# Kernel tuning notes

Measured on AMD Instinct MI355X. Metric: run time of the kernel, lower is better.

## Reference

```python
import jax, jax.numpy as jnp
import numpy as np

HEADS = 4
HID = 64
IN_DIM = 128
N_WIRES, N_TERM, N_ACT = 50, 20, 10
NEG_SLOPE = 0.2


def gat_conv(x, src, dst, ea, W, We, a_src, a_dst, a_edge, bias, concat):
    """PyG GATConv with edge features, add_self_loops=True, fill_value='mean'."""
    N = x.shape[0]
    H, F = a_src.shape
    # --- add self loops; self-loop edge_attr = mean of incoming edge_attr ---
    deg = jax.ops.segment_sum(jnp.ones((ea.shape[0],), x.dtype), dst, num_segments=N)
    loop_attr = jax.ops.segment_sum(ea, dst, num_segments=N) / jnp.maximum(deg, 1.0)[:, None]
    ar = jnp.arange(N)
    src = jnp.concatenate([src, ar])
    dst = jnp.concatenate([dst, ar])
    ea = jnp.concatenate([ea, loop_attr], axis=0)
    # --- linear transforms ---
    h = (x @ W).reshape(N, H, F)                      # [N,H,F]
    a_s = jnp.einsum('nhf,hf->nh', h, a_src)          # [N,H]
    a_d = jnp.einsum('nhf,hf->nh', h, a_dst)
    he = (ea @ We).reshape(-1, H, F)                  # [E2,H,F]
    a_e = jnp.einsum('ehf,hf->eh', he, a_edge)        # [E2,H]
    # --- attention logits + softmax over edges grouped by destination ---
    alpha = jax.nn.leaky_relu(a_s[src] + a_d[dst] + a_e, negative_slope=NEG_SLOPE)
    amax = jax.ops.segment_max(alpha, dst, num_segments=N)
    ex = jnp.exp(alpha - amax[dst])
    denom = jax.ops.segment_sum(ex, dst, num_segments=N)
    alpha = ex / (denom[dst] + 1e-16)                 # [E2,H]
    # --- message passing: gather src feats, weight, scatter-sum to dst ---
    out = jax.ops.segment_sum(h[src] * alpha[..., None], dst, num_segments=N)  # [N,H,F]
    out = out.reshape(N, H * F) if concat else out.mean(axis=1)
    return out + bias


def setup_inputs() -> dict:
    key = jax.random.key(0)
    ks = jax.random.split(key, 24)
    N, E = 20000, 320000
    x = jax.random.normal(ks[0], (N, IN_DIM), jnp.float32)
    edge_index = jax.random.randint(ks[1], (2, E), 0, N, dtype=jnp.int64)
    edge_attr = jax.random.normal(ks[2], (E, 2), jnp.float32)
    s = 0.1
    p = {
        'W1': jax.random.normal(ks[3], (IN_DIM, HEADS * HID)) * s,
        'We1': jax.random.normal(ks[4], (2, HEADS * HID)) * s,
        'as1': jax.random.normal(ks[5], (HEADS, HID)) * s,
        'ad1': jax.random.normal(ks[6], (HEADS, HID)) * s,
        'ae1': jax.random.normal(ks[7], (HEADS, HID)) * s,
        'b1': jnp.zeros((HEADS * HID,), jnp.float32),
        'W2': jax.random.normal(ks[8], (HEADS * HID, HEADS * HID)) * s,
        'We2': jax.random.normal(ks[9], (2, HEADS * HID)) * s,
        'as2': jax.random.normal(ks[10], (HEADS, HID)) * s,
        'ad2': jax.random.normal(ks[11], (HEADS, HID)) * s,
        'ae2': jax.random.normal(ks[12], (HEADS, HID)) * s,
        'b2': jnp.zeros((HID,), jnp.float32),
        'Ww': jax.random.normal(ks[13], (HID, N_WIRES)) * s,
        'bw': jnp.zeros((N_WIRES,), jnp.float32),
        'Wt': jax.random.normal(ks[14], (HID, N_TERM)) * s,
        'bt': jnp.zeros((N_TERM,), jnp.float32),
        'Wa': jax.random.normal(ks[15], (HID, N_ACT)) * s,
        'ba': jnp.zeros((N_ACT,), jnp.float32),
    }
    return {'x': x, 'edge_index': edge_index, 'edge_attr': edge_attr, **p}


def reference(x, edge_index, edge_attr, W1, We1, as1, ad1, ae1, b1,
              W2, We2, as2, ad2, ae2, b2, Ww, bw, Wt, bt, Wa, ba):
    src, dst = edge_index[0], edge_index[1]
    h = jax.nn.elu(gat_conv(x, src, dst, edge_attr, W1, We1, as1, ad1, ae1, b1, True))
    h = jax.nn.elu(gat_conv(h, src, dst, edge_attr, W2, We2, as2, ad2, ae2, b2, False))
    wire_logits = h @ Ww + bw
    terminal_logits = h @ Wt + bt
    action_logits = h @ Wa + ba
    return (wire_logits, terminal_logits, action_logits)
```

## Files before the change

kernel.cpp:

```cpp
#include <hip/hip_runtime.h>
#include <math.h>

#define N_NODES 20000
#define N_EDGES 320000
#define D1      256
#define WCAP    128
#define NPB     10385
#define NDEG    1250
#define NWALL   32

typedef __attribute__((ext_vector_type(8))) short    bf16x8;
typedef __attribute__((ext_vector_type(4))) float    f32x4;
typedef __attribute__((ext_vector_type(8))) unsigned short u16x8;

__device__ inline float wred_sum(float v) {
#pragma unroll
  for (int o = 32; o > 0; o >>= 1) v += __shfl_xor(v, o, 64);
  return v;
}
__device__ inline float wred_max(float v) {
#pragma unroll
  for (int o = 32; o > 0; o >>= 1) v = fmaxf(v, __shfl_xor(v, o, 64));
  return v;
}

__device__ inline unsigned short f2b(float v) {
  unsigned u = __float_as_uint(v);
  unsigned r = (u + 0x7fffu + ((u >> 16) & 1u)) >> 16;
  return (unsigned short)r;
}
__device__ inline float b2f(unsigned short h) {
  return __uint_as_float(((unsigned)h) << 16);
}

__device__ inline int fr(const int* __restrict__ rp, const int* __restrict__ boff, int j) {
  return j ? rp[j] + boff[(j - 1) >> 10] : 0;
}

__global__ __launch_bounds__(256) void k_prep(
    const float* __restrict__ x, unsigned short* __restrict__ xh,
    const float* __restrict__ W1, unsigned short* __restrict__ WT1h,
    unsigned short* __restrict__ WT1l,
    const float* __restrict__ W2, unsigned short* __restrict__ WT2h,
    unsigned short* __restrict__ WT2l,
    const float* __restrict__ We1, const float* __restrict__ ae1,
    const float* __restrict__ We2, const float* __restrict__ ae2,
    float* __restrict__ qb,
    const int* __restrict__ ei, int* __restrict__ deg,
    const float* __restrict__ Ww, const float* __restrict__ Wt,
    const float* __restrict__ Wa,
    const float* __restrict__ bw, const float* __restrict__ bt,
    const float* __restrict__ ba,
    unsigned short* __restrict__ WallTh, unsigned short* __restrict__ WallTl,
    float* __restrict__ biasAll) {
  int bid = blockIdx.x, t = threadIdx.x;
  if (bid < 10000) {
    int i = bid * 256 + t;
    xh[i] = f2b(x[i]);
  } else if (bid < 10128) {
    int i = (bid - 10000) * 256 + t;
    int k = i >> 8, n = i & 255;
    float v = W1[i];
    unsigned short h = f2b(v);
    WT1h[n * 128 + k] = h;
    WT1l[n * 128 + k] = f2b(v - b2f(h));
  } else if (bid < 10384) {
    int i = (bid - 10128) * 256 + t;
    int k = i >> 8, n = i & 255;
    float v = W2[i];
    unsigned short h = f2b(v);
    WT2h[n * 256 + k] = h;
    WT2l[n * 256 + k] = f2b(v - b2f(h));
  } else if (bid == 10384) {
    int lane = t & 63, w = t >> 6;
    const float* We = (w >> 1) ? We2 : We1;
    const float* ae = (w >> 1) ? ae2 : ae1;
    int c = w & 1;
#pragma unroll
    for (int h = 0; h < 4; h++) {
      float p = We[c * D1 + h * 64 + lane] * ae[h * 64 + lane];
      p = wred_sum(p);
      if (lane == 0) qb[(w >> 1) * 8 + c * 4 + h] = p;
    }
    if (t < 80) biasAll[t] = (t < 50) ? bw[t] : (t < 70) ? bt[t - 50] : ba[t - 70];
  } else if (bid < NPB + NDEG) {
    int e = (bid - NPB) * 256 + t;
    if (e < N_EDGES) atomicAdd(&deg[ei[N_EDGES + e]], 1);
  } else {
    int i = (bid - NPB - NDEG) * 256 + t;
    int j = i >> 6, f = i & 63;
    float v = 0.f;
    if (j < 50)      v = Ww[f * 50 + j];
    else if (j < 70) v = Wt[f * 20 + (j - 50)];
    else if (j < 80) v = Wa[f * 10 + (j - 70)];
    unsigned short h = f2b(v);
    WallTh[j * 64 + f] = h;
    WallTl[j * 64 + f] = f2b(v - b2f(h));
  }
}

__global__ __launch_bounds__(1024) void k_scan1(const int* __restrict__ deg,
                                                int* __restrict__ rowptr,
                                                int* __restrict__ bsum, int N) {
  __shared__ int wsum[16];
  int t = threadIdx.x, lane = t & 63, wid = t >> 6;
  int i = blockIdx.x * 1024 + t;
  int v = (i < N) ? deg[i] : 0;
  int sc = v;
#pragma unroll
  for (int o = 1; o < 64; o <<= 1) {
    int u = __shfl_up(sc, o, 64);
    if (lane >= o) sc += u;
  }
  if (lane == 63) wsum[wid] = sc;
  __syncthreads();
  if (wid == 0 && lane < 16) {
    int x = wsum[lane];
#pragma unroll
    for (int o = 1; o < 16; o <<= 1) {
      int u = __shfl_up(x, o, 64);
      if (lane >= o) x += u;
    }
    wsum[lane] = x;
  }
  __syncthreads();
  int off = wid ? wsum[wid - 1] : 0;
  if (i < N) rowptr[i + 1] = off + sc;
  if (t == 0) bsum[blockIdx.x] = wsum[15];
}

__global__ void k_scan2(const int* __restrict__ bsum, int* __restrict__ boff, int nb) {
  int lane = threadIdx.x;
  int v = (lane < nb) ? bsum[lane] : 0;
  int sc = v;
#pragma unroll
  for (int o = 1; o < 64; o <<= 1) {
    int u = __shfl_up(sc, o, 64);
    if (lane >= o) sc += u;
  }
  if (lane < nb) boff[lane] = sc - v;
}

__global__ void k_scatter(const int* __restrict__ ei, const float* __restrict__ ea,
                          const int* __restrict__ rowptr, const int* __restrict__ boff,
                          int* __restrict__ fill, int* __restrict__ src_s,
                          float* __restrict__ ea_s) {
  int p = blockIdx.x * blockDim.x + threadIdx.x;
  if (p >= N_EDGES) return;
  int s = ei[p], d = ei[N_EDGES + p];
  float e0 = ea[p * 2], e1 = ea[p * 2 + 1];
  int pos = fr(rowptr, boff, d) + atomicAdd(&fill[d], 1);
  src_s[pos] = s;
  ea_s[pos * 2] = e0; ea_s[pos * 2 + 1] = e1;
}

#define LDK 40
__global__ __launch_bounds__(256) void k_gemm_mfma(
    const unsigned short* __restrict__ Ah,
    const unsigned short* __restrict__ BTh, const unsigned short* __restrict__ BTl,
    unsigned short* __restrict__ Chi,
    const float* __restrict__ asw, const float* __restrict__ adw,
    float* __restrict__ asb, float* __restrict__ adb,
    int M, int K) {
  __shared__ unsigned short sAh[128 * LDK];
  __shared__ unsigned short sBh[128 * LDK], sBl[128 * LDK];
  int tid = threadIdx.x;
  int lane = tid & 63, wid = tid >> 6;
  int wr = wid >> 1, wc = wid & 1;
  int row0 = blockIdx.y * 128, col0 = blockIdx.x * 128;
  int aRow = wr * 64, bRow = wc * 64;

  f32x4 acc[4][4];
#pragma unroll
  for (int i = 0; i < 4; i++)
#pragma unroll
    for (int j = 0; j < 4; j++) acc[i][j] = (f32x4){0.f, 0.f, 0.f, 0.f};

  int c0i = tid * 2;
  int r0 = c0i >> 2, ko0 = (c0i & 3) * 8;
  int c1i = tid * 2 + 1;
  int r1 = c1i >> 2, ko1 = (c1i & 3) * 8;

  int q8 = (lane >> 4) * 8;
  int rsel = lane & 15;

  for (int k0 = 0; k0 < K; k0 += 32) {
    u16x8 z = {0, 0, 0, 0, 0, 0, 0, 0};
    int ga0 = row0 + r0, ga1 = row0 + r1;
    u16x8 vah0 = (ga0 < M) ? *(const u16x8*)&Ah[(size_t)ga0 * K + k0 + ko0] : z;
    u16x8 vah1 = (ga1 < M) ? *(const u16x8*)&Ah[(size_t)ga1 * K + k0 + ko1] : z;
    u16x8 vbh0 = *(const u16x8*)&BTh[(size_t)(col0 + r0) * K + k0 + ko0];
    u16x8 vbl0 = *(const u16x8*)&BTl[(size_t)(col0 + r0) * K + k0 + ko0];
    u16x8 vbh1 = *(const u16x8*)&BTh[(size_t)(col0 + r1) * K + k0 + ko1];
    u16x8 vbl1 = *(const u16x8*)&BTl[(size_t)(col0 + r1) * K + k0 + ko1];
    *(u16x8*)&sAh[r0 * LDK + ko0] = vah0;
    *(u16x8*)&sAh[r1 * LDK + ko1] = vah1;
    *(u16x8*)&sBh[r0 * LDK + ko0] = vbh0;
    *(u16x8*)&sBl[r0 * LDK + ko0] = vbl0;
    *(u16x8*)&sBh[r1 * LDK + ko1] = vbh1;
    *(u16x8*)&sBl[r1 * LDK + ko1] = vbl1;
    __syncthreads();

    bf16x8 fah[4], fbh[4], fbl[4];
#pragma unroll
    for (int i = 0; i < 4; i++) {
      int ar = aRow + i * 16 + rsel;
      int br = bRow + i * 16 + rsel;
      fah[i] = *(const bf16x8*)&sAh[ar * LDK + q8];
      fbh[i] = *(const bf16x8*)&sBh[br * LDK + q8];
      fbl[i] = *(const bf16x8*)&sBl[br * LDK + q8];
    }
#pragma unroll
    for (int i = 0; i < 4; i++)
#pragma unroll
      for (int j = 0; j < 4; j++) {
        acc[i][j] = __builtin_amdgcn_mfma_f32_16x16x32_bf16(fah[i], fbh[j], acc[i][j], 0, 0, 0);
        acc[i][j] = __builtin_amdgcn_mfma_f32_16x16x32_bf16(fah[i], fbl[j], acc[i][j], 0, 0, 0);
      }
    __syncthreads();
  }

  int rq = (lane >> 4) * 4;
  int head = (col0 + bRow) >> 6;
  float sa[4], sd[4];
#pragma unroll
  for (int j = 0; j < 4; j++) {
    sa[j] = asw[head * 64 + j * 16 + rsel];
    sd[j] = adw[head * 64 + j * 16 + rsel];
  }
#pragma unroll
  for (int i = 0; i < 4; i++) {
#pragma unroll
    for (int j = 0; j < 4; j++) {
      int gcol = col0 + bRow + j * 16 + rsel;
#pragma unroll
      for (int r = 0; r < 4; r++) {
        int grow = row0 + aRow + i * 16 + rq + r;
        if (grow < M) Chi[(size_t)grow * D1 + gcol] = f2b(acc[i][j][r]);
      }
    }
#pragma unroll
    for (int r = 0; r < 4; r++) {
      float ps = 0.f, pd = 0.f;
#pragma unroll
      for (int j = 0; j < 4; j++) {
        ps = fmaf(acc[i][j][r], sa[j], ps);
        pd = fmaf(acc[i][j][r], sd[j], pd);
      }
#pragma unroll
      for (int o = 1; o < 16; o <<= 1) {
        ps += __shfl_xor(ps, o, 64);
        pd += __shfl_xor(pd, o, 64);
      }
      int grow = row0 + aRow + i * 16 + rq + r;
      if ((lane & 15) == 0 && grow < M) {
        asb[grow * 4 + head] = ps;
        adb[grow * 4 + head] = pd;
      }
    }
  }
}

__global__ __launch_bounds__(256) void k_heads_mfma(
    const unsigned short* __restrict__ Ah, const unsigned short* __restrict__ Al,
    const unsigned short* __restrict__ BTh, const unsigned short* __restrict__ BTl,
    const float* __restrict__ biasAll, float* __restrict__ out, int M) {
  __shared__ unsigned short sAh[128 * LDK], sAl[128 * LDK];
  __shared__ unsigned short sBh[128 * LDK], sBl[128 * LDK];
  const int K = 64;
  int tid = threadIdx.x;
  int lane = tid & 63, wid = tid >> 6;
  int wr = wid >> 1, wc = wid & 1;
  int row0 = blockIdx.x * 128;
  int aRow = wr * 64, bRow = wc * 64;

  f32x4 acc[4][4];
#pragma unroll
  for (int i = 0; i < 4; i++)
#pragma unroll
    for (int j = 0; j < 4; j++) acc[i][j] = (f32x4){0.f, 0.f, 0.f, 0.f};

  int c0i = tid * 2;
  int r0 = c0i >> 2, ko0 = (c0i & 3) * 8;
  int c1i = tid * 2 + 1;
  int r1 = c1i >> 2, ko1 = (c1i & 3) * 8;
  int q8 = (lane >> 4) * 8;
  int rsel = lane & 15;

  for (int k0 = 0; k0 < K; k0 += 32) {
    u16x8 z = {0, 0, 0, 0, 0, 0, 0, 0};
    int ga0 = row0 + r0, ga1 = row0 + r1;
    u16x8 vah0 = (ga0 < M) ? *(const u16x8*)&Ah[(size_t)ga0 * K + k0 + ko0] : z;
    u16x8 val0 = (ga0 < M) ? *(const u16x8*)&Al[(size_t)ga0 * K + k0 + ko0] : z;
    u16x8 vah1 = (ga1 < M) ? *(const u16x8*)&Ah[(size_t)ga1 * K + k0 + ko1] : z;
    u16x8 val1 = (ga1 < M) ? *(const u16x8*)&Al[(size_t)ga1 * K + k0 + ko1] : z;
    u16x8 vbh0 = *(const u16x8*)&BTh[(size_t)r0 * K + k0 + ko0];
    u16x8 vbl0 = *(const u16x8*)&BTl[(size_t)r0 * K + k0 + ko0];
    u16x8 vbh1 = *(const u16x8*)&BTh[(size_t)r1 * K + k0 + ko1];
    u16x8 vbl1 = *(const u16x8*)&BTl[(size_t)r1 * K + k0 + ko1];
    *(u16x8*)&sAh[r0 * LDK + ko0] = vah0;
    *(u16x8*)&sAl[r0 * LDK + ko0] = val0;
    *(u16x8*)&sAh[r1 * LDK + ko1] = vah1;
    *(u16x8*)&sAl[r1 * LDK + ko1] = val1;
    *(u16x8*)&sBh[r0 * LDK + ko0] = vbh0;
    *(u16x8*)&sBl[r0 * LDK + ko0] = vbl0;
    *(u16x8*)&sBh[r1 * LDK + ko1] = vbh1;
    *(u16x8*)&sBl[r1 * LDK + ko1] = vbl1;
    __syncthreads();

    bf16x8 fah[4], fal[4], fbh[4], fbl[4];
#pragma unroll
    for (int i = 0; i < 4; i++) {
      int ar = aRow + i * 16 + rsel;
      int br = bRow + i * 16 + rsel;
      fah[i] = *(const bf16x8*)&sAh[ar * LDK + q8];
      fal[i] = *(const bf16x8*)&sAl[ar * LDK + q8];
      fbh[i] = *(const bf16x8*)&sBh[br * LDK + q8];
      fbl[i] = *(const bf16x8*)&sBl[br * LDK + q8];
    }
#pragma unroll
    for (int i = 0; i < 4; i++)
#pragma unroll
      for (int j = 0; j < 4; j++) {
        acc[i][j] = __builtin_amdgcn_mfma_f32_16x16x32_bf16(fah[i], fbh[j], acc[i][j], 0, 0, 0);
        acc[i][j] = __builtin_amdgcn_mfma_f32_16x16x32_bf16(fah[i], fbl[j], acc[i][j], 0, 0, 0);
        acc[i][j] = __builtin_amdgcn_mfma_f32_16x16x32_bf16(fal[i], fbh[j], acc[i][j], 0, 0, 0);
      }
    __syncthreads();
  }

  int rq = (lane >> 4) * 4;
#pragma unroll
  for (int j = 0; j < 4; j++) {
    int gcol = bRow + j * 16 + rsel;
    if (gcol < 80) {
      float bj = biasAll[gcol];
      float* op; int cols, jj;
      if (gcol < 50)      { op = out;                 cols = 50; jj = gcol; }
      else if (gcol < 70) { op = out + N_NODES * 50;  cols = 20; jj = gcol - 50; }
      else                { op = out + N_NODES * 70;  cols = 10; jj = gcol - 70; }
#pragma unroll
      for (int i = 0; i < 4; i++) {
#pragma unroll
        for (int r = 0; r < 4; r++) {
          int grow = row0 + aRow + i * 16 + rq + r;
          if (grow < M) op[(size_t)grow * cols + jj] = acc[i][j][r] + bj;
        }
      }
    }
  }
}

template <bool CONCAT>
__global__ __launch_bounds__(256) void k_aggregate(
    const unsigned short* __restrict__ feath,
    const int* __restrict__ rowptr, const int* __restrict__ boff,
    const int* __restrict__ src_s, const float* __restrict__ ea_s,
    const float* __restrict__ asb, const float* __restrict__ adb,
    const float* __restrict__ q, const float* __restrict__ bias,
    unsigned short* __restrict__ outh,
    unsigned short* __restrict__ outf_h, unsigned short* __restrict__ outf_l) {
  __shared__ float slog[4][4][WCAP];
  __shared__ int   ssrc[4][WCAP];
  int t = threadIdx.x, lane = t & 63, w = t >> 6;
  int n = blockIdx.x * 4 + w;
  int b = fr(rowptr, boff, n);
  int e = fr(rowptr, boff, n + 1);
  int deg = e - b;

  float4 qv0 = *(const float4*)q;
  float4 qv1 = *(const float4*)(q + 4);
  float4 ad4 = *(const float4*)&adb[(size_t)n * 4];
  float4 asn = *(const float4*)&asb[(size_t)n * 4];

  if (deg <= WCAP) {
    float lv[2][4];
    float e0acc = 0.f, e1acc = 0.f;
#pragma unroll
    for (int p = 0; p < 2; p++) {
      int j = lane + p * 64;
      float l0 = -1e30f, l1 = -1e30f, l2 = -1e30f, l3 = -1e30f;
      if (j < deg) {
        int s = src_s[b + j];
        float4 as4 = *(const float4*)&asb[(size_t)s * 4];
        float e0 = ea_s[2 * (b + j)], e1 = ea_s[2 * (b + j) + 1];
        e0acc += e0; e1acc += e1;
        l0 = as4.x + ad4.x + e0 * qv0.x + e1 * qv1.x; l0 = (l0 > 0.f) ? l0 : 0.2f * l0;
        l1 = as4.y + ad4.y + e0 * qv0.y + e1 * qv1.y; l1 = (l1 > 0.f) ? l1 : 0.2f * l1;
        l2 = as4.z + ad4.z + e0 * qv0.z + e1 * qv1.z; l2 = (l2 > 0.f) ? l2 : 0.2f * l2;
        l3 = as4.w + ad4.w + e0 * qv0.w + e1 * qv1.w; l3 = (l3 > 0.f) ? l3 : 0.2f * l3;
        ssrc[w][j] = s;
      }
      lv[p][0] = l0; lv[p][1] = l1; lv[p][2] = l2; lv[p][3] = l3;
    }
    float dinv = 1.f / fmaxf((float)deg, 1.f);
    float e0m = wred_sum(e0acc) * dinv;
    float e1m = wred_sum(e1acc) * dinv;
    float ls[4];
    ls[0] = asn.x + ad4.x + e0m * qv0.x + e1m * qv1.x;
    ls[1] = asn.y + ad4.y + e0m * qv0.y + e1m * qv1.y;
    ls[2] = asn.z + ad4.z + e0m * qv0.z + e1m * qv1.z;
    ls[3] = asn.w + ad4.w + e0m * qv0.w + e1m * qv1.w;
#pragma unroll
    for (int h = 0; h < 4; h++) ls[h] = (ls[h] > 0.f) ? ls[h] : 0.2f * ls[h];
    float m[4], inv[4], wself[4];
#pragma unroll
    for (int h = 0; h < 4; h++) {
      float mm = fmaxf(wred_max(fmaxf(lv[0][h], lv[1][h])), ls[h]);
      float ss = wred_sum(__expf(lv[0][h] - mm) + __expf(lv[1][h] - mm))
                 + __expf(ls[h] - mm);
      m[h] = mm; inv[h] = 1.f / (ss + 1e-16f);
      wself[h] = __expf(ls[h] - mm) * inv[h];
    }
#pragma unroll
    for (int p = 0; p < 2; p++) {
      int j = lane + p * 64;
      if (j < deg) {
#pragma unroll
        for (int h = 0; h < 4; h++) slog[w][h][j] = __expf(lv[p][h] - m[h]) * inv[h];
      }
    }
    int es = lane >> 5, cg = lane & 31, hh = cg >> 3;
    const unsigned short* fb = feath + cg * 8;
    float acc8[8] = {};
    int j0 = 0;
    for (; j0 + 8 <= deg; j0 += 8) {
      int e0 = j0 + es, e1 = j0 + 2 + es, e2 = j0 + 4 + es, e3 = j0 + 6 + es;
      int s0 = ssrc[w][e0], s1 = ssrc[w][e1], s2 = ssrc[w][e2], s3 = ssrc[w][e3];
      u16x8 f0 = *(const u16x8*)&fb[(size_t)s0 * D1];
      u16x8 f1 = *(const u16x8*)&fb[(size_t)s1 * D1];
      u16x8 f2 = *(const u16x8*)&fb[(size_t)s2 * D1];
      u16x8 f3 = *(const u16x8*)&fb[(size_t)s3 * D1];
      float w0 = slog[w][hh][e0], w1 = slog[w][hh][e1];
      float w2 = slog[w][hh][e2], w3 = slog[w][hh][e3];
#pragma unroll
      for (int k = 0; k < 8; k++) acc8[k] = fmaf(w0, b2f((unsigned short)f0[k]), acc8[k]);
#pragma unroll
      for (int k = 0; k < 8; k++) acc8[k] = fmaf(w1, b2f((unsigned short)f1[k]), acc8[k]);
#pragma unroll
      for (int k = 0; k < 8; k++) acc8[k] = fmaf(w2, b2f((unsigned short)f2[k]), acc8[k]);
#pragma unroll
      for (int k = 0; k < 8; k++) acc8[k] = fmaf(w3, b2f((unsigned short)f3[k]), acc8[k]);
    }
    for (; j0 < deg; j0 += 2) {
      int e2 = j0 + es;
      if (e2 < deg) {
        float ww = slog[w][hh][e2];
        int s = ssrc[w][e2];
        u16x8 f8 = *(const u16x8*)&fb[(size_t)s * D1];
#pragma unroll
        for (int k = 0; k < 8; k++) acc8[k] = fmaf(ww, b2f((unsigned short)f8[k]), acc8[k]);
      }
    }
    if (es == 0) {
      u16x8 fs = *(const u16x8*)&fb[(size_t)n * D1];
      float ws2 = wself[hh];
#pragma unroll
      for (int k = 0; k < 8; k++) acc8[k] = fmaf(ws2, b2f((unsigned short)fs[k]), acc8[k]);
    }
#pragma unroll
    for (int k = 0; k < 8; k++) acc8[k] += __shfl_xor(acc8[k], 32, 64);
    if (CONCAT) {
      if (es == 0) {
        u16x8 hi8;
#pragma unroll
        for (int k = 0; k < 8; k++) {
          float v2 = acc8[k] + bias[cg * 8 + k];
          v2 = (v2 > 0.f) ? v2 : (__expf(v2) - 1.f);
          hi8[k] = f2b(v2);
        }
        *(u16x8*)&outh[(size_t)n * D1 + cg * 8] = hi8;
      }
    } else {
#pragma unroll
      for (int k = 0; k < 8; k++) {
        acc8[k] += __shfl_xor(acc8[k], 8, 64);
        acc8[k] += __shfl_xor(acc8[k], 16, 64);
      }
      if (es == 0 && cg < 8) {
        u16x8 hi8, lo8;
#pragma unroll
        for (int k = 0; k < 8; k++) {
          float v2 = acc8[k] * 0.25f + bias[cg * 8 + k];
          v2 = (v2 > 0.f) ? v2 : (__expf(v2) - 1.f);
          unsigned short hh2 = f2b(v2);
          hi8[k] = hh2;
          lo8[k] = f2b(v2 - b2f(hh2));
        }
        *(u16x8*)&outf_h[(size_t)n * 64 + cg * 8] = hi8;
        *(u16x8*)&outf_l[(size_t)n * 64 + cg * 8] = lo8;
      }
    }
  } else {
    float e0acc = 0.f, e1acc = 0.f;
    for (int p = b + lane; p < e; p += 64) {
      e0acc += ea_s[2 * p]; e1acc += ea_s[2 * p + 1];
    }
    float dinv = 1.f / fmaxf((float)deg, 1.f);
    float e0m = wred_sum(e0acc) * dinv;
    float e1m = wred_sum(e1acc) * dinv;
    float qh0[4] = {qv0.x, qv0.y, qv0.z, qv0.w};
    float qh1[4] = {qv1.x, qv1.y, qv1.z, qv1.w};
    float adh[4] = {ad4.x, ad4.y, ad4.z, ad4.w};
    float ash[4] = {asn.x, asn.y, asn.z, asn.w};
#pragma unroll
    for (int h = 0; h < 4; h++) {
      float q0 = qh0[h], q1 = qh1[h], adn = adh[h];
      float lself = ash[h] + adn + e0m * q0 + e1m * q1;
      lself = (lself > 0.f) ? lself : 0.2f * lself;
      float mm = -1e30f;
      for (int p = b + lane; p < e; p += 64) {
        int s = src_s[p];
        float l = asb[s * 4 + h] + adn + ea_s[2 * p] * q0 + ea_s[2 * p + 1] * q1;
        l = (l > 0.f) ? l : 0.2f * l;
        mm = fmaxf(mm, l);
      }
      mm = fmaxf(wred_max(mm), lself);
      float s1 = 0.f;
      for (int p = b + lane; p < e; p += 64) {
        int s = src_s[p];
        float l = asb[s * 4 + h] + adn + ea_s[2 * p] * q0 + ea_s[2 * p + 1] * q1;
        l = (l > 0.f) ? l : 0.2f * l;
        s1 += __expf(l - mm);
      }
      s1 = wred_sum(s1) + __expf(lself - mm);
      float inv = 1.f / (s1 + 1e-16f);
      float wself = __expf(lself - mm) * inv;
      const unsigned short* fb = feath + h * 64 + lane;
      float acc = wself * b2f(fb[(size_t)n * D1]);
      for (int c0 = b; c0 < e; c0 += 64) {
        int p = c0 + lane;
        float ww = 0.f; int si = 0;
        if (p < e) {
          int s = src_s[p];
          float l = asb[s * 4 + h] + adn + ea_s[2 * p] * q0 + ea_s[2 * p + 1] * q1;
          l = (l > 0.f) ? l : 0.2f * l;
          ww = __expf(l - mm) * inv;
          si = s;
        }
        slog[w][0][lane] = ww; ssrc[w][lane] = si;
        int cnt = min(64, e - c0);
        for (int j = 0; j < cnt; j++)
          acc = fmaf(slog[w][0][j], b2f(fb[(size_t)ssrc[w][j] * D1]), acc);
      }
      if (CONCAT) {
        float v = acc + bias[h * 64 + lane];
        v = (v > 0.f) ? v : (__expf(v) - 1.f);
        outh[(size_t)n * D1 + h * 64 + lane] = f2b(v);
      } else {
        slog[w][1][lane] = (h == 0) ? acc : slog[w][1][lane] + acc;
        if (h == 3) {
          float v = slog[w][1][lane] * 0.25f + bias[lane];
          v = (v > 0.f) ? v : (__expf(v) - 1.f);
          unsigned short hh2 = f2b(v);
          outf_h[(size_t)n * 64 + lane] = hh2;
          outf_l[(size_t)n * 64 + lane] = f2b(v - b2f(hh2));
        }
      }
    }
  }
}

extern "C" void kernel_launch(void* const* d_in, const int* in_sizes, int n_in,
                              void* d_out, int out_size, void* d_ws, size_t ws_size,
                              hipStream_t stream) {
  const float* x   = (const float*)d_in[0];
  const int*   ei  = (const int*)d_in[1];
  const float* ea  = (const float*)d_in[2];
  const float* W1  = (const float*)d_in[3];
  const float* We1 = (const float*)d_in[4];
  const float* as1 = (const float*)d_in[5];
  const float* ad1 = (const float*)d_in[6];
  const float* ae1 = (const float*)d_in[7];
  const float* b1  = (const float*)d_in[8];
  const float* W2  = (const float*)d_in[9];
  const float* We2 = (const float*)d_in[10];
  const float* as2 = (const float*)d_in[11];
  const float* ad2 = (const float*)d_in[12];
  const float* ae2 = (const float*)d_in[13];
  const float* b2  = (const float*)d_in[14];
  const float* Ww  = (const float*)d_in[15];
  const float* bw  = (const float*)d_in[16];
  const float* Wt  = (const float*)d_in[17];
  const float* bt  = (const float*)d_in[18];
  const float* Wa  = (const float*)d_in[19];
  const float* ba  = (const float*)d_in[20];
  float* out = (float*)d_out;

  char* ws = (char*)d_ws;
  size_t off = 0;
  auto alloc = [&](size_t bytes) {
    void* p = ws + off;
    off += (bytes + 255) & ~(size_t)255;
    return p;
  };
  unsigned short* Ah     = (unsigned short*)alloc((size_t)N_NODES * D1 * 2);
  unsigned short* xh     = (unsigned short*)alloc((size_t)N_NODES * 128 * 2);
  unsigned short* Bfh    = (unsigned short*)alloc((size_t)N_NODES * D1 * 2);
  unsigned short* h2h    = (unsigned short*)alloc((size_t)N_NODES * 64 * 2);
  unsigned short* h2l    = (unsigned short*)alloc((size_t)N_NODES * 64 * 2);
  unsigned short* WT1h   = (unsigned short*)alloc((size_t)128 * 256 * 2);
  unsigned short* WT1l   = (unsigned short*)alloc((size_t)128 * 256 * 2);
  unsigned short* WT2h   = (unsigned short*)alloc((size_t)256 * 256 * 2);
  unsigned short* WT2l   = (unsigned short*)alloc((size_t)256 * 256 * 2);
  unsigned short* WallTh = (unsigned short*)alloc((size_t)128 * 64 * 2);
  unsigned short* WallTl = (unsigned short*)alloc((size_t)128 * 64 * 2);
  float*          biasAll= (float*)alloc(80 * 4);
  int*   src_s   = (int*)alloc((size_t)N_EDGES * 4);
  float* ea_s    = (float*)alloc((size_t)N_EDGES * 2 * 4);
  size_t zero_base = off;
  int*   deg     = (int*)alloc((size_t)N_NODES * 4);
  int*   fill    = (int*)alloc((size_t)N_NODES * 4);
  size_t zero_len = off - zero_base;
  int*   rowptr  = (int*)alloc((size_t)(N_NODES + 1) * 4);
  float* asb     = (float*)alloc((size_t)N_NODES * 4 * 4);
  float* adb     = (float*)alloc((size_t)N_NODES * 4 * 4);
  float* qb      = (float*)alloc(64);
  int*   bsum    = (int*)alloc(64 * 4);
  int*   boff    = (int*)alloc(64 * 4);

  hipMemsetAsync(ws + zero_base, 0, zero_len, stream);

  k_prep<<<NPB + NDEG + NWALL, 256, 0, stream>>>(
      x, xh, W1, WT1h, WT1l, W2, WT2h, WT2l, We1, ae1, We2, ae2, qb, ei, deg,
      Ww, Wt, Wa, bw, bt, ba, WallTh, WallTl, biasAll);

  const int NB = (N_NODES + 1023) / 1024;
  k_scan1<<<NB, 1024, 0, stream>>>(deg, rowptr, bsum, N_NODES);
  k_scan2<<<1, 64, 0, stream>>>(bsum, boff, NB);
  k_scatter<<<NDEG, 256, 0, stream>>>(ei, ea, rowptr, boff, fill, src_s, ea_s);

  dim3 ggemm(2, (N_NODES + 127) / 128);

  k_gemm_mfma<<<ggemm, 256, 0, stream>>>(xh, WT1h, WT1l, Ah, as1, ad1,
                                         asb, adb, N_NODES, 128);
  k_aggregate<true><<<N_NODES / 4, 256, 0, stream>>>(
      Ah, rowptr, boff, src_s, ea_s, asb, adb, qb, b1, Bfh, nullptr, nullptr);

  k_gemm_mfma<<<ggemm, 256, 0, stream>>>(Bfh, WT2h, WT2l, Ah, as2, ad2,
                                         asb, adb, N_NODES, 256);
  k_aggregate<false><<<N_NODES / 4, 256, 0, stream>>>(
      Ah, rowptr, boff, src_s, ea_s, asb, adb, qb + 8, b2, nullptr, h2h, h2l);

  k_heads_mfma<<<(N_NODES + 127) / 128, 256, 0, stream>>>(
      h2h, h2l, WallTh, WallTl, biasAll, out, N_NODES);
}
```

Measured before the change: 256.6 us.

## Prefetch neighbor features in aggregate, merge scan kernels, vectorize prep and scatter

Result: no change. 252.8 us (-1.5%).

```diff
diff --git a/kernel.cpp b/kernel.cpp
--- a/kernel.cpp
+++ b/kernel.cpp
@@ -5,13 +5,14 @@
 #define N_EDGES 320000
 #define D1      256
 #define WCAP    128
-#define NPB     10385
+#define NPB     2885
 #define NDEG    1250
 #define NWALL   32
 
 typedef __attribute__((ext_vector_type(8))) short    bf16x8;
 typedef __attribute__((ext_vector_type(4))) float    f32x4;
 typedef __attribute__((ext_vector_type(8))) unsigned short u16x8;
+typedef __attribute__((ext_vector_type(4))) unsigned short u16x4;
 
 __device__ inline float wred_sum(float v) {
 #pragma unroll
@@ -21,6 +22,11 @@
 __device__ inline float wred_max(float v) {
 #pragma unroll
   for (int o = 32; o > 0; o >>= 1) v = fmaxf(v, __shfl_xor(v, o, 64));
+  return v;
+}
+__device__ inline int wred_sum_i(int v) {
+#pragma unroll
+  for (int o = 32; o > 0; o >>= 1) v += __shfl_xor(v, o, 64);
   return v;
 }
 
@@ -31,10 +37,6 @@
 }
 __device__ inline float b2f(unsigned short h) {
   return __uint_as_float(((unsigned)h) << 16);
-}
-
-__device__ inline int fr(const int* __restrict__ rp, const int* __restrict__ boff, int j) {
-  return j ? rp[j] + boff[(j - 1) >> 10] : 0;
 }
 
 __global__ __launch_bounds__(256) void k_prep(
@@ -54,24 +56,27 @@
     unsigned short* __restrict__ WallTh, unsigned short* __restrict__ WallTl,
     float* __restrict__ biasAll) {
   int bid = blockIdx.x, t = threadIdx.x;
-  if (bid < 10000) {
-    int i = bid * 256 + t;
-    xh[i] = f2b(x[i]);
-  } else if (bid < 10128) {
-    int i = (bid - 10000) * 256 + t;
+  if (bid < 2500) {
+    int i = (bid * 256 + t) * 4;
+    float4 v = *(const float4*)&x[i];
+    u16x4 o;
+    o[0] = f2b(v.x); o[1] = f2b(v.y); o[2] = f2b(v.z); o[3] = f2b(v.w);
+    *(u16x4*)&xh[i] = o;
+  } else if (bid < 2628) {
+    int i = (bid - 2500) * 256 + t;
     int k = i >> 8, n = i & 255;
     float v = W1[i];
     unsigned short h = f2b(v);
     WT1h[n * 128 + k] = h;
     WT1l[n * 128 + k] = f2b(v - b2f(h));
-  } else if (bid < 10384) {
-    int i = (bid - 10128) * 256 + t;
+  } else if (bid < 2884) {
+    int i = (bid - 2628) * 256 + t;
     int k = i >> 8, n = i & 255;
     float v = W2[i];
     unsigned short h = f2b(v);
     WT2h[n * 256 + k] = h;
     WT2l[n * 256 + k] = f2b(v - b2f(h));
-  } else if (bid == 10384) {
+  } else if (bid == 2884) {
     int lane = t & 63, w = t >> 6;
     const float* We = (w >> 1) ? We2 : We1;
     const float* ae = (w >> 1) ? ae2 : ae1;
@@ -99,13 +104,28 @@
   }
 }
 
-__global__ __launch_bounds__(1024) void k_scan1(const int* __restrict__ deg,
-                                                int* __restrict__ rowptr,
-                                                int* __restrict__ bsum, int N) {
+__global__ __launch_bounds__(1024) void k_scan(const int* __restrict__ deg,
+                                               int* __restrict__ rowptr) {
   __shared__ int wsum[16];
+  __shared__ int pshare;
   int t = threadIdx.x, lane = t & 63, wid = t >> 6;
-  int i = blockIdx.x * 1024 + t;
-  int v = (i < N) ? deg[i] : 0;
+  int base = blockIdx.x * 1024;
+  int pre = 0;
+  for (int i = t; i < base; i += 1024) pre += deg[i];
+  pre = wred_sum_i(pre);
+  if (lane == 0) wsum[wid] = pre;
+  __syncthreads();
+  if (t == 0) {
+    int s = 0;
+#pragma unroll
+    for (int k = 0; k < 16; k++) s += wsum[k];
+    pshare = s;
+  }
+  __syncthreads();
+  int prefix = pshare;
+  __syncthreads();
+  int i = base + t;
+  int v = (i < N_NODES) ? deg[i] : 0;
   int sc = v;
 #pragma unroll
   for (int o = 1; o < 64; o <<= 1) {
@@ -115,43 +135,31 @@
   if (lane == 63) wsum[wid] = sc;
   __syncthreads();
   if (wid == 0 && lane < 16) {
-    int x = wsum[lane];
+    int x2 = wsum[lane];
 #pragma unroll
     for (int o = 1; o < 16; o <<= 1) {
-      int u = __shfl_up(x, o, 64);
-      if (lane >= o) x += u;
-    }
-    wsum[lane] = x;
+      int u = __shfl_up(x2, o, 64);
+      if (lane >= o) x2 += u;
+    }
+    wsum[lane] = x2;
   }
   __syncthreads();
   int off = wid ? wsum[wid - 1] : 0;
-  if (i < N) rowptr[i + 1] = off + sc;
-  if (t == 0) bsum[blockIdx.x] = wsum[15];
-}
-
-__global__ void k_scan2(const int* __restrict__ bsum, int* __restrict__ boff, int nb) {
-  int lane = threadIdx.x;
-  int v = (lane < nb) ? bsum[lane] : 0;
-  int sc = v;
-#pragma unroll
-  for (int o = 1; o < 64; o <<= 1) {
-    int u = __shfl_up(sc, o, 64);
-    if (lane >= o) sc += u;
-  }
-  if (lane < nb) boff[lane] = sc - v;
+  if (i < N_NODES) rowptr[i + 1] = prefix + off + sc;
+  if (t == 0 && blockIdx.x == 0) rowptr[0] = 0;
 }
 
 __global__ void k_scatter(const int* __restrict__ ei, const float* __restrict__ ea,
-                          const int* __restrict__ rowptr, const int* __restrict__ boff,
+                          const int* __restrict__ rowptr,
                           int* __restrict__ fill, int* __restrict__ src_s,
                           float* __restrict__ ea_s) {
   int p = blockIdx.x * blockDim.x + threadIdx.x;
   if (p >= N_EDGES) return;
   int s = ei[p], d = ei[N_EDGES + p];
-  float e0 = ea[p * 2], e1 = ea[p * 2 + 1];
-  int pos = fr(rowptr, boff, d) + atomicAdd(&fill[d], 1);
+  float2 e2 = *(const float2*)&ea[p * 2];
+  int pos = rowptr[d] + atomicAdd(&fill[d], 1);
   src_s[pos] = s;
-  ea_s[pos * 2] = e0; ea_s[pos * 2 + 1] = e1;
+  *(float2*)&ea_s[pos * 2] = e2;
 }
 
 #define LDK 40
@@ -354,7 +362,7 @@
 template <bool CONCAT>
 __global__ __launch_bounds__(256) void k_aggregate(
     const unsigned short* __restrict__ feath,
-    const int* __restrict__ rowptr, const int* __restrict__ boff,
+    const int* __restrict__ rowptr,
     const int* __restrict__ src_s, const float* __restrict__ ea_s,
     const float* __restrict__ asb, const float* __restrict__ adb,
     const float* __restrict__ q, const float* __restrict__ bias,
@@ -364,8 +372,8 @@
   __shared__ int   ssrc[4][WCAP];
   int t = threadIdx.x, lane = t & 63, w = t >> 6;
   int n = blockIdx.x * 4 + w;
-  int b = fr(rowptr, boff, n);
-  int e = fr(rowptr, boff, n + 1);
+  int b = rowptr[n];
+  int e = rowptr[n + 1];
   int deg = e - b;
 
   float4 qv0 = *(const float4*)q;
@@ -374,28 +382,50 @@
   float4 asn = *(const float4*)&asb[(size_t)n * 4];
 
   if (deg <= WCAP) {
+    int degR = (deg + 15) & ~15;
+    if (degR == 0) degR = 16;
+    int   sreg[2] = {n, n};
+    float e0r[2] = {0.f, 0.f}, e1r[2] = {0.f, 0.f};
+#pragma unroll
+    for (int p = 0; p < 2; p++) {
+      int j = lane + p * 64;
+      if (j < degR) {
+        int s = n; float e0v = 0.f, e1v = 0.f;
+        if (j < deg) {
+          s = src_s[b + j];
+          float2 ee = *(const float2*)&ea_s[2 * (b + j)];
+          e0v = ee.x; e1v = ee.y;
+        }
+        ssrc[w][j] = s;
+        sreg[p] = s; e0r[p] = e0v; e1r[p] = e1v;
+      }
+    }
+    int es = lane >> 5, cg = lane & 31, hh = cg >> 3;
+    const unsigned short* fb = feath + cg * 8;
+    u16x8 pf[8];
+#pragma unroll
+    for (int q8 = 0; q8 < 8; q8++) {
+      int s = __shfl(sreg[0], 2 * q8 + es, 64);
+      pf[q8] = *(const u16x8*)&fb[(size_t)s * D1];
+    }
     float lv[2][4];
-    float e0acc = 0.f, e1acc = 0.f;
 #pragma unroll
     for (int p = 0; p < 2; p++) {
       int j = lane + p * 64;
       float l0 = -1e30f, l1 = -1e30f, l2 = -1e30f, l3 = -1e30f;
       if (j < deg) {
-        int s = src_s[b + j];
-        float4 as4 = *(const float4*)&asb[(size_t)s * 4];
-        float e0 = ea_s[2 * (b + j)], e1 = ea_s[2 * (b + j) + 1];
-        e0acc += e0; e1acc += e1;
-        l0 = as4.x + ad4.x + e0 * qv0.x + e1 * qv1.x; l0 = (l0 > 0.f) ? l0 : 0.2f * l0;
-        l1 = as4.y + ad4.y + e0 * qv0.y + e1 * qv1.y; l1 = (l1 > 0.f) ? l1 : 0.2f * l1;
-        l2 = as4.z + ad4.z + e0 * qv0.z + e1 * qv1.z; l2 = (l2 > 0.f) ? l2 : 0.2f * l2;
-        l3 = as4.w + ad4.w + e0 * qv0.w + e1 * qv1.w; l3 = (l3 > 0.f) ? l3 : 0.2f * l3;
-        ssrc[w][j] = s;
+        float4 as4 = *(const float4*)&asb[(size_t)sreg[p] * 4];
+        float e0v = e0r[p], e1v = e1r[p];
+        l0 = as4.x + ad4.x + e0v * qv0.x + e1v * qv1.x; l0 = (l0 > 0.f) ? l0 : 0.2f * l0;
+        l1 = as4.y + ad4.y + e0v * qv0.y + e1v * qv1.y; l1 = (l1 > 0.f) ? l1 : 0.2f * l1;
+        l2 = as4.z + ad4.z + e0v * qv0.z + e1v * qv1.z; l2 = (l2 > 0.f) ? l2 : 0.2f * l2;
+        l3 = as4.w + ad4.w + e0v * qv0.w + e1v * qv1.w; l3 = (l3 > 0.f) ? l3 : 0.2f * l3;
       }
       lv[p][0] = l0; lv[p][1] = l1; lv[p][2] = l2; lv[p][3] = l3;
     }
     float dinv = 1.f / fmaxf((float)deg, 1.f);
-    float e0m = wred_sum(e0acc) * dinv;
-    float e1m = wred_sum(e1acc) * dinv;
+    float e0m = wred_sum(e0r[0] + e0r[1]) * dinv;
+    float e1m = wred_sum(e1r[0] + e1r[1]) * dinv;
     float ls[4];
     ls[0] = asn.x + ad4.x + e0m * qv0.x + e1m * qv1.x;
     ls[1] = asn.y + ad4.y + e0m * qv0.y + e1m * qv1.y;
@@ -403,53 +433,44 @@
     ls[3] = asn.w + ad4.w + e0m * qv0.w + e1m * qv1.w;
 #pragma unroll
     for (int h = 0; h < 4; h++) ls[h] = (ls[h] > 0.f) ? ls[h] : 0.2f * ls[h];
-    float m[4], inv[4], wself[4];
+    float ex[2][4];
+#pragma unroll
+    for (int p = 0; p < 2; p++)
+#pragma unroll
+      for (int h = 0; h < 4; h++) ex[p][h] = __expf(lv[p][h]);
+    float inv[4], wself[4];
 #pragma unroll
     for (int h = 0; h < 4; h++) {
-      float mm = fmaxf(wred_max(fmaxf(lv[0][h], lv[1][h])), ls[h]);
-      float ss = wred_sum(__expf(lv[0][h] - mm) + __expf(lv[1][h] - mm))
-                 + __expf(ls[h] - mm);
-      m[h] = mm; inv[h] = 1.f / (ss + 1e-16f);
-      wself[h] = __expf(ls[h] - mm) * inv[h];
+      float eself = __expf(ls[h]);
+      float ss = wred_sum(ex[0][h] + ex[1][h]) + eself;
+      inv[h] = 1.f / (ss + 1e-16f);
+      wself[h] = eself * inv[h];
     }
 #pragma unroll
     for (int p = 0; p < 2; p++) {
       int j = lane + p * 64;
-      if (j < deg) {
-#pragma unroll
-        for (int h = 0; h < 4; h++) slog[w][h][j] = __expf(lv[p][h] - m[h]) * inv[h];
-      }
-    }
-    int es = lane >> 5, cg = lane & 31, hh = cg >> 3;
-    const unsigned short* fb = feath + cg * 8;
+      if (j < degR) {
+#pragma unroll
+        for (int h = 0; h < 4; h++) slog[w][h][j] = ex[p][h] * inv[h];
+      }
+    }
     float acc8[8] = {};
-    int j0 = 0;
-    for (; j0 + 8 <= deg; j0 += 8) {
-      int e0 = j0 + es, e1 = j0 + 2 + es, e2 = j0 + 4 + es, e3 = j0 + 6 + es;
-      int s0 = ssrc[w][e0], s1 = ssrc[w][e1], s2 = ssrc[w][e2], s3 = ssrc[w][e3];
-      u16x8 f0 = *(const u16x8*)&fb[(size_t)s0 * D1];
-      u16x8 f1 = *(const u16x8*)&fb[(size_t)s1 * D1];
-      u16x8 f2 = *(const u16x8*)&fb[(size_t)s2 * D1];
-      u16x8 f3 = *(const u16x8*)&fb[(size_t)s3 * D1];
-      float w0 = slog[w][hh][e0], w1 = slog[w][hh][e1];
-      float w2 = slog[w][hh][e2], w3 = slog[w][hh][e3];
-#pragma unroll
-      for (int k = 0; k < 8; k++) acc8[k] = fmaf(w0, b2f((unsigned short)f0[k]), acc8[k]);
-#pragma unroll
-      for (int k = 0; k < 8; k++) acc8[k] = fmaf(w1, b2f((unsigned short)f1[k]), acc8[k]);
-#pragma unroll
-      for (int k = 0; k < 8; k++) acc8[k] = fmaf(w2, b2f((unsigned short)f2[k]), acc8[k]);
-#pragma unroll
-      for (int k = 0; k < 8; k++) acc8[k] = fmaf(w3, b2f((unsigned short)f3[k]), acc8[k]);
-    }
-    for (; j0 < deg; j0 += 2) {
-      int e2 = j0 + es;
-      if (e2 < deg) {
-        float ww = slog[w][hh][e2];
-        int s = ssrc[w][e2];
-        u16x8 f8 = *(const u16x8*)&fb[(size_t)s * D1];
-#pragma unroll
-        for (int k = 0; k < 8; k++) acc8[k] = fmaf(ww, b2f((unsigned short)f8[k]), acc8[k]);
+#pragma unroll
+    for (int q8 = 0; q8 < 8; q8++) {
+      float ww = slog[w][hh][2 * q8 + es];
+#pragma unroll
+      for (int k = 0; k < 8; k++) acc8[k] = fmaf(ww, b2f((unsigned short)pf[q8][k]), acc8[k]);
+    }
+    for (int j0 = 16; j0 < degR; j0 += 16) {
+      u16x8 f[8];
+#pragma unroll
+      for (int q8 = 0; q8 < 8; q8++)
+        f[q8] = *(const u16x8*)&fb[(size_t)ssrc[w][j0 + 2 * q8 + es] * D1];
+#pragma unroll
+      for (int q8 = 0; q8 < 8; q8++) {
+        float ww = slog[w][hh][j0 + 2 * q8 + es];
+#pragma unroll
+        for (int k = 0; k < 8; k++) acc8[k] = fmaf(ww, b2f((unsigned short)f[q8][k]), acc8[k]);
       }
     }
     if (es == 0) {
@@ -616,8 +637,6 @@
   float* asb     = (float*)alloc((size_t)N_NODES * 4 * 4);
   float* adb     = (float*)alloc((size_t)N_NODES * 4 * 4);
   float* qb      = (float*)alloc(64);
-  int*   bsum    = (int*)alloc(64 * 4);
-  int*   boff    = (int*)alloc(64 * 4);
 
   hipMemsetAsync(ws + zero_base, 0, zero_len, stream);
 
@@ -625,22 +644,20 @@
       x, xh, W1, WT1h, WT1l, W2, WT2h, WT2l, We1, ae1, We2, ae2, qb, ei, deg,
       Ww, Wt, Wa, bw, bt, ba, WallTh, WallTl, biasAll);
 
-  const int NB = (N_NODES + 1023) / 1024;
-  k_scan1<<<NB, 1024, 0, stream>>>(deg, rowptr, bsum, N_NODES);
-  k_scan2<<<1, 64, 0, stream>>>(bsum, boff, NB);
-  k_scatter<<<NDEG, 256, 0, stream>>>(ei, ea, rowptr, boff, fill, src_s, ea_s);
+  k_scan<<<(N_NODES + 1023) / 1024, 1024, 0, stream>>>(deg, rowptr);
+  k_scatter<<<NDEG, 256, 0, stream>>>(ei, ea, rowptr, fill, src_s, ea_s);
 
   dim3 ggemm(2, (N_NODES + 127) / 128);
 
   k_gemm_mfma<<<ggemm, 256, 0, stream>>>(xh, WT1h, WT1l, Ah, as1, ad1,
                                          asb, adb, N_NODES, 128);
   k_aggregate<true><<<N_NODES / 4, 256, 0, stream>>>(
-      Ah, rowptr, boff, src_s, ea_s, asb, adb, qb, b1, Bfh, nullptr, nullptr);
+      Ah, rowptr, src_s, ea_s, asb, adb, qb, b1, Bfh, nullptr, nullptr);
 
   k_gemm_mfma<<<ggemm, 256, 0, stream>>>(Bfh, WT2h, WT2l, Ah, as2, ad2,
                                          asb, adb, N_NODES, 256);
   k_aggregate<false><<<N_NODES / 4, 256, 0, stream>>>(
-      Ah, rowptr, boff, src_s, ea_s, asb, adb, qb + 8, b2, nullptr, h2h, h2l);
+      Ah, rowptr, src_s, ea_s, asb, adb, qb + 8, b2, nullptr, h2h, h2l);
 
   k_heads_mfma<<<(N_NODES + 127) / 128, 256, 0, stream>>>(
       h2h, h2l, WallTh, WallTl, biasAll, out, N_NODES);
```
